# Kernel tuning notes

Hardware: AMD Instinct MI355X
Metric: run time of the kernel (lower is better)

Reference implementation:

```python
import jax, jax.numpy as jnp
import numpy as np

BATCH, FLAT_IN, PROJ_DIM, HEADS, ACT_DIM = 2048, 512, 256, 16384, 64


def setup_inputs() -> dict:
    key = jax.random.key(0)
    k1, k2, k3, k4 = jax.random.split(key, 4)
    state = jax.random.normal(k1, (BATCH, FLAT_IN), dtype=jnp.float32)
    random_projection = jax.random.normal(k2, (FLAT_IN, PROJ_DIM), dtype=jnp.float32)
    memories = jax.random.normal(k3, (HEADS, PROJ_DIM), dtype=jnp.float32)
    logits = jax.random.normal(k4, (HEADS, ACT_DIM), dtype=jnp.float32)
    return {"state": state, "random_projection": random_projection,
            "memories": memories, "logits": logits}


def reference(state, random_projection, memories, logits):
    # state: [B, flat_in] -> projected [B, proj_dim] (proj_dim branch of __call__)
    s = state.reshape(state.shape[0], -1) @ random_projection
    # sum(state[:,None] * memories[None,:], -1) == dot-product similarity GEMM
    similarities = jnp.einsum('bd,hd->bh', s, memories)  # [B, heads]
    closest = jnp.argmax(similarities, axis=1)           # [B]
    return logits[closest]                                # [B, act_dim]
```

## Files before the change

### kernel.cpp

```cpp
#include <hip/hip_runtime.h>

#define BATCH    2048
#define FLAT_IN  512
#define PROJ_DIM 256
#define HEADS    16384
#define ACT_DIM  64

typedef __attribute__((ext_vector_type(8))) short short8;
typedef _Float16 half8 __attribute__((ext_vector_type(8)));
typedef __attribute__((ext_vector_type(4))) float floatx4;

__device__ __forceinline__ unsigned short f2bf(float x) {
  unsigned u = __float_as_uint(x);
  u += 0x7fff + ((u >> 16) & 1);
  return (unsigned short)(u >> 16);
}
__device__ __forceinline__ float bf2f(unsigned short b) {
  return __uint_as_float(((unsigned)b) << 16);
}
__device__ __forceinline__ unsigned short f2h(float x) {
  _Float16 h = (_Float16)x;
  return __builtin_bit_cast(unsigned short, h);
}

__device__ __forceinline__ void top2_ins(float v, int h, float& b1, int& i1,
                                         float& b2, int& i2) {
  if (v > b1 || (v == b1 && h < i1)) { b2 = b1; i2 = i1; b1 = v; i1 = h; }
  else if (v > b2 || (v == b2 && h < i2)) { b2 = v; i2 = h; }
}

#define GLDS16(g, l)                                                          \
  __builtin_amdgcn_global_load_lds(                                           \
      (__attribute__((address_space(1))) void*)(void*)(g),                    \
      (__attribute__((address_space(3))) void*)(l), 16, 0, 0)

__global__ __launch_bounds__(256) void prep(
    const float* __restrict__ state, const float* __restrict__ rp,
    const float* __restrict__ mem,
    unsigned short* __restrict__ st_hi, unsigned short* __restrict__ st_mid,
    unsigned short* __restrict__ rpT_hi, unsigned short* __restrict__ rpT_mid,
    unsigned short* __restrict__ mem_f16)
{
  const int tid = threadIdx.x;
  const int b = blockIdx.x;
  if (b < 1024) {
    int i = b * 256 + tid;
    float4 v = ((const float4*)state)[i];
    ushort4 h, m;
    h.x = f2bf(v.x); m.x = f2bf(v.x - bf2f(h.x));
    h.y = f2bf(v.y); m.y = f2bf(v.y - bf2f(h.y));
    h.z = f2bf(v.z); m.z = f2bf(v.z - bf2f(h.z));
    h.w = f2bf(v.w); m.w = f2bf(v.w - bf2f(h.w));
    ((ushort4*)st_hi)[i]  = h;
    ((ushort4*)st_mid)[i] = m;
  } else if (b < 1056) {
    __shared__ float t[64][65];
    int bid = b - 1024;
    int k0 = (bid >> 2) * 64, n0 = (bid & 3) * 64;
#pragma unroll
    for (int it = 0; it < 16; ++it) {
      int lin = it * 256 + tid;
      int kr = lin >> 6, nc = lin & 63;
      t[kr][nc] = rp[(size_t)(k0 + kr) * PROJ_DIM + n0 + nc];
    }
    __syncthreads();
#pragma unroll
    for (int it = 0; it < 16; ++it) {
      int lin = it * 256 + tid;
      int nr = lin >> 6, kc = lin & 63;
      float v = t[kc][nr];
      unsigned short hh = f2bf(v);
      rpT_hi [(size_t)(n0 + nr) * FLAT_IN + k0 + kc] = hh;
      rpT_mid[(size_t)(n0 + nr) * FLAT_IN + k0 + kc] = f2bf(v - bf2f(hh));
    }
  } else {
    int i2 = (b - 1056) * 256 + tid;
    float4 x = ((const float4*)mem)[2 * i2];
    float4 y = ((const float4*)mem)[2 * i2 + 1];
    short8 o;
    o[0] = (short)f2h(x.x); o[1] = (short)f2h(x.y);
    o[2] = (short)f2h(x.z); o[3] = (short)f2h(x.w);
    o[4] = (short)f2h(y.x); o[5] = (short)f2h(y.y);
    o[6] = (short)f2h(y.z); o[7] = (short)f2h(y.w);
    ((short8*)mem_f16)[i2] = o;
  }
}

__global__ __launch_bounds__(256, 2) void gemm_proj(
    const unsigned short* __restrict__ Ahi, const unsigned short* __restrict__ Amid,
    const unsigned short* __restrict__ Bhi, const unsigned short* __restrict__ Bmid,
    float* __restrict__ S, unsigned short* __restrict__ Sf16)
{
  __shared__ __align__(16) unsigned short sm[4][64 * 64];
  const int tid = threadIdx.x;
  const int lane = tid & 63, w = tid >> 6;
  const int quad = lane >> 4, col = lane & 15;
  const int wm = (w >> 1) * 32, wn = (w & 1) * 32;
  const int m0 = blockIdx.x * 64, n0 = blockIdx.y * 64;

  floatx4 acc[2][2];
#pragma unroll
  for (int i = 0; i < 2; ++i)
#pragma unroll
    for (int j = 0; j < 2; ++j) {
      acc[i][j][0] = 0.f; acc[i][j][1] = 0.f;
      acc[i][j][2] = 0.f; acc[i][j][3] = 0.f;
    }

  const int P0 = tid, P1 = tid + 256;
  const int r0 = P0 >> 3, kl0 = (P0 & 7) ^ (r0 & 7);
  const int r1 = P1 >> 3, kl1 = (P1 & 7) ^ (r1 & 7);

  for (int kc = 0; kc < FLAT_IN; kc += 64) {
    GLDS16(Ahi  + (size_t)(m0 + r0) * FLAT_IN + kc + kl0 * 8, &sm[0][P0 * 8]);
    GLDS16(Ahi  + (size_t)(m0 + r1) * FLAT_IN + kc + kl1 * 8, &sm[0][P1 * 8]);
    GLDS16(Amid + (size_t)(m0 + r0) * FLAT_IN + kc + kl0 * 8, &sm[1][P0 * 8]);
    GLDS16(Amid + (size_t)(m0 + r1) * FLAT_IN + kc + kl1 * 8, &sm[1][P1 * 8]);
    GLDS16(Bhi  + (size_t)(n0 + r0) * FLAT_IN + kc + kl0 * 8, &sm[2][P0 * 8]);
    GLDS16(Bhi  + (size_t)(n0 + r1) * FLAT_IN + kc + kl1 * 8, &sm[2][P1 * 8]);
    GLDS16(Bmid + (size_t)(n0 + r0) * FLAT_IN + kc + kl0 * 8, &sm[3][P0 * 8]);
    GLDS16(Bmid + (size_t)(n0 + r1) * FLAT_IN + kc + kl1 * 8, &sm[3][P1 * 8]);
    __syncthreads();

#pragma unroll
    for (int ks = 0; ks < 2; ++ks) {
      short8 bf[2][2];
#pragma unroll
      for (int j = 0; j < 2; ++j) {
        int rr = wn + j * 16 + col;
        int off = rr * 64 + (((ks * 4 + quad) ^ (rr & 7)) * 8);
        bf[j][0] = *(const short8*)&sm[2][off];
        bf[j][1] = *(const short8*)&sm[3][off];
      }
#pragma unroll
      for (int i = 0; i < 2; ++i) {
        int rr = wm + i * 16 + col;
        int off = rr * 64 + (((ks * 4 + quad) ^ (rr & 7)) * 8);
        short8 a0 = *(const short8*)&sm[0][off];
        short8 a1 = *(const short8*)&sm[1][off];
#pragma unroll
        for (int j = 0; j < 2; ++j) {
          acc[i][j] = __builtin_amdgcn_mfma_f32_16x16x32_bf16(a0, bf[j][0], acc[i][j], 0, 0, 0);
          acc[i][j] = __builtin_amdgcn_mfma_f32_16x16x32_bf16(a0, bf[j][1], acc[i][j], 0, 0, 0);
          acc[i][j] = __builtin_amdgcn_mfma_f32_16x16x32_bf16(a1, bf[j][0], acc[i][j], 0, 0, 0);
        }
      }
    }
    __syncthreads();
  }

#pragma unroll
  for (int i = 0; i < 2; ++i)
#pragma unroll
    for (int j = 0; j < 2; ++j)
#pragma unroll
      for (int r = 0; r < 4; ++r) {
        int row = m0 + wm + i * 16 + quad * 4 + r;
        int c   = n0 + wn + j * 16 + col;
        float v = acc[i][j][r];
        S   [(size_t)row * PROJ_DIM + c] = v;
        Sf16[(size_t)row * PROJ_DIM + c] = f2h(v);
      }
}

__global__ __launch_bounds__(512, 4) void sim_topk(
    const unsigned short* __restrict__ Af16,
    const unsigned short* __restrict__ Bf16,
    float4* __restrict__ partial)
{
  __shared__ __align__(16) unsigned short smA[128 * 64];
  __shared__ __align__(16) unsigned short smB[256 * 64];
  const int tid = threadIdx.x;
  const int lane = tid & 63, w = tid >> 6;
  const int quad = lane >> 4, col = lane & 15;
  const int wm = (w >> 2) * 64, wn = (w & 3) * 64;
  const int m0 = blockIdx.x * 128;
  const int h0 = blockIdx.y * 256;

  floatx4 acc[4][4];
#pragma unroll
  for (int i = 0; i < 4; ++i)
#pragma unroll
    for (int j = 0; j < 4; ++j) {
      acc[i][j][0] = 0.f; acc[i][j][1] = 0.f;
      acc[i][j][2] = 0.f; acc[i][j][3] = 0.f;
    }

  const int PA0 = tid, PA1 = tid + 512;
  const int ra0 = PA0 >> 3, ka0 = (PA0 & 7) ^ (ra0 & 7);
  const int ra1 = PA1 >> 3, ka1 = (PA1 & 7) ^ (ra1 & 7);
  int rb[4], kb[4];
#pragma unroll
  for (int t = 0; t < 4; ++t) {
    int P = t * 512 + tid;
    rb[t] = P >> 3; kb[t] = (P & 7) ^ (rb[t] & 7);
  }

  for (int kc = 0; kc < PROJ_DIM; kc += 64) {
    GLDS16(Af16 + (size_t)(m0 + ra0) * PROJ_DIM + kc + ka0 * 8, &smA[PA0 * 8]);
    GLDS16(Af16 + (size_t)(m0 + ra1) * PROJ_DIM + kc + ka1 * 8, &smA[PA1 * 8]);
#pragma unroll
    for (int t = 0; t < 4; ++t) {
      GLDS16(Bf16 + (size_t)(h0 + rb[t]) * PROJ_DIM + kc + kb[t] * 8,
             &smB[(t * 512 + tid) * 8]);
    }
    __syncthreads();

#pragma unroll
    for (int ks = 0; ks < 2; ++ks) {
      half8 a[4], bfr[4];
#pragma unroll
      for (int i = 0; i < 4; ++i) {
        int rr = wm + i * 16 + col;
        int off = rr * 64 + (((ks * 4 + quad) ^ (rr & 7)) * 8);
        a[i] = *(const half8*)&smA[off];
      }
#pragma unroll
      for (int j = 0; j < 4; ++j) {
        int rr = wn + j * 16 + col;
        int off = rr * 64 + (((ks * 4 + quad) ^ (rr & 7)) * 8);
        bfr[j] = *(const half8*)&smB[off];
      }
#pragma unroll
      for (int i = 0; i < 4; ++i)
#pragma unroll
        for (int j = 0; j < 4; ++j)
          acc[i][j] = __builtin_amdgcn_mfma_f32_16x16x32_f16(a[i], bfr[j], acc[i][j], 0, 0, 0);
    }
    __syncthreads();
  }

  float4* lds_p = (float4*)smA;

#pragma unroll
  for (int i = 0; i < 4; ++i)
#pragma unroll
    for (int r = 0; r < 4; ++r) {
      float b1 = acc[i][0][r]; int h1 = h0 + wn + col;
      float b2 = -3.4e38f;     int h2 = h1;
#pragma unroll
      for (int j = 1; j < 4; ++j) {
        float v = acc[i][j][r]; int h = h0 + wn + j * 16 + col;
        if (v > b1) { b2 = b1; h2 = h1; b1 = v; h1 = h; }
        else if (v > b2) { b2 = v; h2 = h; }
      }
#pragma unroll
      for (int m = 1; m <= 8; m <<= 1) {
        float ob1 = __shfl_xor(b1, m); int oh1 = __shfl_xor(h1, m);
        float ob2 = __shfl_xor(b2, m); int oh2 = __shfl_xor(h2, m);
        if (ob1 > b1) {
          if (b1 > ob2) { b2 = b1;  h2 = h1;  }
          else          { b2 = ob2; h2 = oh2; }
          b1 = ob1; h1 = oh1;
        } else if (ob1 > b2) { b2 = ob1; h2 = oh1; }
      }
      if (col == 0) {
        int row = wm + i * 16 + quad * 4 + r;
        lds_p[row * 4 + (w & 3)] =
            make_float4(b1, __int_as_float(h1), b2, __int_as_float(h2));
      }
    }
  __syncthreads();

  if (tid < 128) {
    int row = tid;
    float b1 = -3.4e38f, b2 = -3.4e38f; int h1 = 0x7fffffff, h2 = 0x7fffffff;
#pragma unroll
    for (int t = 0; t < 4; ++t) {
      float4 p = lds_p[row * 4 + t];
      top2_ins(p.x, __float_as_int(p.y), b1, h1, b2, h2);
      top2_ins(p.z, __float_as_int(p.w), b1, h1, b2, h2);
    }
    partial[(size_t)(m0 + row) * 64 + blockIdx.y] =
        make_float4(b1, __int_as_float(h1), b2, __int_as_float(h2));
  }
}

__global__ __launch_bounds__(64) void finalize(
    const float4* __restrict__ partial, const float* __restrict__ S,
    const float* __restrict__ Mem, const float* __restrict__ logits,
    float* __restrict__ out)
{
  const int row  = blockIdx.x;
  const int lane = threadIdx.x;

  float4 p = partial[(size_t)row * 64 + lane];
  float v0 = p.x; int c0 = __float_as_int(p.y);
  float v1 = p.z; int c1 = __float_as_int(p.w);

  int cand[4];
#pragma unroll
  for (int t = 0; t < 4; ++t) {
    float lv; int lh;
    if (v0 > v1 || (v0 == v1 && c0 < c1)) { lv = v0; lh = c0; }
    else                                  { lv = v1; lh = c1; }
#pragma unroll
    for (int d = 32; d; d >>= 1) {
      float ov = __shfl_xor(lv, d); int oh = __shfl_xor(lh, d);
      if (ov > lv || (ov == lv && oh < lh)) { lv = ov; lh = oh; }
    }
    cand[t] = lh;
    if (c0 == lh) v0 = -3.4e38f;
    if (c1 == lh) v1 = -3.4e38f;
  }

  float4 sv = ((const float4*)(S + (size_t)row * PROJ_DIM))[lane];
  float bestv = -3.4e38f; int besth = 0x7fffffff;
#pragma unroll
  for (int t = 0; t < 4; ++t) {
    float4 mv = ((const float4*)(Mem + (size_t)cand[t] * PROJ_DIM))[lane];
    float d = sv.x * mv.x + sv.y * mv.y + sv.z * mv.z + sv.w * mv.w;
#pragma unroll
    for (int s = 32; s; s >>= 1) d += __shfl_xor(d, s);
    if (d > bestv || (d == bestv && cand[t] < besth)) { bestv = d; besth = cand[t]; }
  }
  out[(size_t)row * ACT_DIM + lane] = logits[(size_t)besth * ACT_DIM + lane];
}

extern "C" void kernel_launch(void* const* d_in, const int* in_sizes, int n_in,
                              void* d_out, int out_size, void* d_ws, size_t ws_size,
                              hipStream_t stream) {
  const float* state  = (const float*)d_in[0];
  const float* rp     = (const float*)d_in[1];
  const float* mem    = (const float*)d_in[2];
  const float* logits = (const float*)d_in[3];
  float* out = (float*)d_out;

  char* ws = (char*)d_ws;
  unsigned short* st_hi   = (unsigned short*)(ws);
  unsigned short* st_mid  = (unsigned short*)(ws + (2u  << 20));
  unsigned short* rpT_hi  = (unsigned short*)(ws + (4u  << 20));
  unsigned short* rpT_mid = (unsigned short*)(ws + (4u  << 20) + (256u << 10));
  unsigned short* mem_f16 = (unsigned short*)(ws + (8u  << 20));
  float*          s       = (float*)(ws + (16u << 20));
  unsigned short* s_f16   = (unsigned short*)(ws + (18u << 20));
  float4*         part    = (float4*)(ws + (20u << 20));

  prep<<<3104, 256, 0, stream>>>(state, rp, mem, st_hi, st_mid,
                                 rpT_hi, rpT_mid, mem_f16);

  gemm_proj<<<dim3(32, 4), 256, 0, stream>>>(st_hi, st_mid, rpT_hi, rpT_mid,
                                             s, s_f16);

  sim_topk<<<dim3(16, 64), 512, 0, stream>>>(s_f16, mem_f16, part);

  finalize<<<BATCH, 64, 0, stream>>>(part, s, mem, logits, out);
}
```

Before: 139.4 us.

## Fuse state split into projection GEMM and register-prefetch tiles in both GEMMs

The bf16 hi/mid split of the state matrix now happens inside gemm_proj, which loads fp32 state directly. This removes a prep pass and its 4 MB round trip through the workspace. Both GEMMs drop the direct global-to-LDS loads in favour of register prefetch of the next K tile overlapped with MFMA work, with a single LDS buffer and extra barriers. sim_topk moves from 512-thread 128x256 tiles to 256-thread 128x128 tiles with a transposed grid, so finalize now merges 128 partials per row instead of 64. This adds register pressure and conversion work inside the GEMM loop.

```diff
diff --git a/kernel.cpp b/kernel.cpp
--- a/kernel.cpp
+++ b/kernel.cpp
@@ -29,52 +29,15 @@
   else if (v > b2 || (v == b2 && h < i2)) { b2 = v; i2 = h; }
 }
 
-#define GLDS16(g, l)                                                          \
-  __builtin_amdgcn_global_load_lds(                                           \
-      (__attribute__((address_space(1))) void*)(void*)(g),                    \
-      (__attribute__((address_space(3))) void*)(l), 16, 0, 0)
-
 __global__ __launch_bounds__(256) void prep(
-    const float* __restrict__ state, const float* __restrict__ rp,
-    const float* __restrict__ mem,
-    unsigned short* __restrict__ st_hi, unsigned short* __restrict__ st_mid,
+    const float* __restrict__ rp, const float* __restrict__ mem,
     unsigned short* __restrict__ rpT_hi, unsigned short* __restrict__ rpT_mid,
     unsigned short* __restrict__ mem_f16)
 {
   const int tid = threadIdx.x;
   const int b = blockIdx.x;
-  if (b < 1024) {
-    int i = b * 256 + tid;
-    float4 v = ((const float4*)state)[i];
-    ushort4 h, m;
-    h.x = f2bf(v.x); m.x = f2bf(v.x - bf2f(h.x));
-    h.y = f2bf(v.y); m.y = f2bf(v.y - bf2f(h.y));
-    h.z = f2bf(v.z); m.z = f2bf(v.z - bf2f(h.z));
-    h.w = f2bf(v.w); m.w = f2bf(v.w - bf2f(h.w));
-    ((ushort4*)st_hi)[i]  = h;
-    ((ushort4*)st_mid)[i] = m;
-  } else if (b < 1056) {
-    __shared__ float t[64][65];
-    int bid = b - 1024;
-    int k0 = (bid >> 2) * 64, n0 = (bid & 3) * 64;
-#pragma unroll
-    for (int it = 0; it < 16; ++it) {
-      int lin = it * 256 + tid;
-      int kr = lin >> 6, nc = lin & 63;
-      t[kr][nc] = rp[(size_t)(k0 + kr) * PROJ_DIM + n0 + nc];
-    }
-    __syncthreads();
-#pragma unroll
-    for (int it = 0; it < 16; ++it) {
-      int lin = it * 256 + tid;
-      int nr = lin >> 6, kc = lin & 63;
-      float v = t[kc][nr];
-      unsigned short hh = f2bf(v);
-      rpT_hi [(size_t)(n0 + nr) * FLAT_IN + k0 + kc] = hh;
-      rpT_mid[(size_t)(n0 + nr) * FLAT_IN + k0 + kc] = f2bf(v - bf2f(hh));
-    }
-  } else {
-    int i2 = (b - 1056) * 256 + tid;
+  if (b < 2048) {
+    int i2 = b * 256 + tid;
     float4 x = ((const float4*)mem)[2 * i2];
     float4 y = ((const float4*)mem)[2 * i2 + 1];
     short8 o;
@@ -83,15 +46,38 @@
     o[4] = (short)f2h(y.x); o[5] = (short)f2h(y.y);
     o[6] = (short)f2h(y.z); o[7] = (short)f2h(y.w);
     ((short8*)mem_f16)[i2] = o;
-  }
-}
-
-__global__ __launch_bounds__(256, 2) void gemm_proj(
-    const unsigned short* __restrict__ Ahi, const unsigned short* __restrict__ Amid,
+  } else {
+    __shared__ float t[64][65];
+    int bid = b - 2048;
+    int k0 = (bid >> 2) * 64, n0 = (bid & 3) * 64;
+#pragma unroll
+    for (int it = 0; it < 16; ++it) {
+      int lin = it * 256 + tid;
+      int kr = lin >> 6, nc = lin & 63;
+      t[kr][nc] = rp[(size_t)(k0 + kr) * PROJ_DIM + n0 + nc];
+    }
+    __syncthreads();
+#pragma unroll
+    for (int it = 0; it < 16; ++it) {
+      int lin = it * 256 + tid;
+      int nr = lin >> 6, kc = lin & 63;
+      float v = t[kc][nr];
+      unsigned short hh = f2bf(v);
+      rpT_hi [(size_t)(n0 + nr) * FLAT_IN + k0 + kc] = hh;
+      rpT_mid[(size_t)(n0 + nr) * FLAT_IN + k0 + kc] = f2bf(v - bf2f(hh));
+    }
+  }
+}
+
+__global__ __launch_bounds__(256, 3) void gemm_proj(
+    const float* __restrict__ state,
     const unsigned short* __restrict__ Bhi, const unsigned short* __restrict__ Bmid,
     float* __restrict__ S, unsigned short* __restrict__ Sf16)
 {
-  __shared__ __align__(16) unsigned short sm[4][64 * 64];
+  __shared__ __align__(16) unsigned short smAhi [64 * 64];
+  __shared__ __align__(16) unsigned short smAmid[64 * 64];
+  __shared__ __align__(16) unsigned short smBhi [64 * 64];
+  __shared__ __align__(16) unsigned short smBmid[64 * 64];
   const int tid = threadIdx.x;
   const int lane = tid & 63, w = tid >> 6;
   const int quad = lane >> 4, col = lane & 15;
@@ -111,17 +97,45 @@
   const int r0 = P0 >> 3, kl0 = (P0 & 7) ^ (r0 & 7);
   const int r1 = P1 >> 3, kl1 = (P1 & 7) ^ (r1 & 7);
 
-  for (int kc = 0; kc < FLAT_IN; kc += 64) {
-    GLDS16(Ahi  + (size_t)(m0 + r0) * FLAT_IN + kc + kl0 * 8, &sm[0][P0 * 8]);
-    GLDS16(Ahi  + (size_t)(m0 + r1) * FLAT_IN + kc + kl1 * 8, &sm[0][P1 * 8]);
-    GLDS16(Amid + (size_t)(m0 + r0) * FLAT_IN + kc + kl0 * 8, &sm[1][P0 * 8]);
-    GLDS16(Amid + (size_t)(m0 + r1) * FLAT_IN + kc + kl1 * 8, &sm[1][P1 * 8]);
-    GLDS16(Bhi  + (size_t)(n0 + r0) * FLAT_IN + kc + kl0 * 8, &sm[2][P0 * 8]);
-    GLDS16(Bhi  + (size_t)(n0 + r1) * FLAT_IN + kc + kl1 * 8, &sm[2][P1 * 8]);
-    GLDS16(Bmid + (size_t)(n0 + r0) * FLAT_IN + kc + kl0 * 8, &sm[3][P0 * 8]);
-    GLDS16(Bmid + (size_t)(n0 + r1) * FLAT_IN + kc + kl1 * 8, &sm[3][P1 * 8]);
-    __syncthreads();
-
+  float4 pa[2][2];
+  float4 pbh[2], pbm[2];
+
+  auto gload = [&](int kc) {
+    const float* a0 = state + (size_t)(m0 + r0) * FLAT_IN + kc + kl0 * 8;
+    const float* a1 = state + (size_t)(m0 + r1) * FLAT_IN + kc + kl1 * 8;
+    pa[0][0] = *(const float4*)a0; pa[0][1] = *(const float4*)(a0 + 4);
+    pa[1][0] = *(const float4*)a1; pa[1][1] = *(const float4*)(a1 + 4);
+    pbh[0] = *(const float4*)(Bhi  + (size_t)(n0 + r0) * FLAT_IN + kc + kl0 * 8);
+    pbh[1] = *(const float4*)(Bhi  + (size_t)(n0 + r1) * FLAT_IN + kc + kl1 * 8);
+    pbm[0] = *(const float4*)(Bmid + (size_t)(n0 + r0) * FLAT_IN + kc + kl0 * 8);
+    pbm[1] = *(const float4*)(Bmid + (size_t)(n0 + r1) * FLAT_IN + kc + kl1 * 8);
+  };
+  auto swrite = [&]() {
+#pragma unroll
+    for (int t = 0; t < 2; ++t) {
+      int P = t ? P1 : P0;
+      float f[8] = {pa[t][0].x, pa[t][0].y, pa[t][0].z, pa[t][0].w,
+                    pa[t][1].x, pa[t][1].y, pa[t][1].z, pa[t][1].w};
+      short8 vh, vm;
+#pragma unroll
+      for (int q = 0; q < 8; ++q) {
+        unsigned short hh = f2bf(f[q]);
+        vh[q] = (short)hh;
+        vm[q] = (short)f2bf(f[q] - bf2f(hh));
+      }
+      *(short8*)&smAhi [P * 8] = vh;
+      *(short8*)&smAmid[P * 8] = vm;
+      *(float4*)&smBhi [P * 8] = pbh[t];
+      *(float4*)&smBmid[P * 8] = pbm[t];
+    }
+  };
+
+  gload(0);
+  swrite();
+  __syncthreads();
+
+  for (int it = 0; it < 8; ++it) {
+    if (it < 7) gload((it + 1) * 64);
 #pragma unroll
     for (int ks = 0; ks < 2; ++ks) {
       short8 bf[2][2];
@@ -129,15 +143,15 @@
       for (int j = 0; j < 2; ++j) {
         int rr = wn + j * 16 + col;
         int off = rr * 64 + (((ks * 4 + quad) ^ (rr & 7)) * 8);
-        bf[j][0] = *(const short8*)&sm[2][off];
-        bf[j][1] = *(const short8*)&sm[3][off];
+        bf[j][0] = *(const short8*)&smBhi [off];
+        bf[j][1] = *(const short8*)&smBmid[off];
       }
 #pragma unroll
       for (int i = 0; i < 2; ++i) {
         int rr = wm + i * 16 + col;
         int off = rr * 64 + (((ks * 4 + quad) ^ (rr & 7)) * 8);
-        short8 a0 = *(const short8*)&sm[0][off];
-        short8 a1 = *(const short8*)&sm[1][off];
+        short8 a0 = *(const short8*)&smAhi [off];
+        short8 a1 = *(const short8*)&smAmid[off];
 #pragma unroll
         for (int j = 0; j < 2; ++j) {
           acc[i][j] = __builtin_amdgcn_mfma_f32_16x16x32_bf16(a0, bf[j][0], acc[i][j], 0, 0, 0);
@@ -147,6 +161,7 @@
       }
     }
     __syncthreads();
+    if (it < 7) { swrite(); __syncthreads(); }
   }
 
 #pragma unroll
@@ -163,19 +178,19 @@
       }
 }
 
-__global__ __launch_bounds__(512, 4) void sim_topk(
+__global__ __launch_bounds__(256, 3) void sim_topk(
     const unsigned short* __restrict__ Af16,
     const unsigned short* __restrict__ Bf16,
     float4* __restrict__ partial)
 {
   __shared__ __align__(16) unsigned short smA[128 * 64];
-  __shared__ __align__(16) unsigned short smB[256 * 64];
+  __shared__ __align__(16) unsigned short smB[128 * 64];
   const int tid = threadIdx.x;
   const int lane = tid & 63, w = tid >> 6;
   const int quad = lane >> 4, col = lane & 15;
-  const int wm = (w >> 2) * 64, wn = (w & 3) * 64;
-  const int m0 = blockIdx.x * 128;
-  const int h0 = blockIdx.y * 256;
+  const int wm = (w >> 1) * 64, wn = (w & 1) * 64;
+  const int h0 = blockIdx.x * 128;
+  const int m0 = blockIdx.y * 128;
 
   floatx4 acc[4][4];
 #pragma unroll
@@ -186,40 +201,48 @@
       acc[i][j][2] = 0.f; acc[i][j][3] = 0.f;
     }
 
-  const int PA0 = tid, PA1 = tid + 512;
-  const int ra0 = PA0 >> 3, ka0 = (PA0 & 7) ^ (ra0 & 7);
-  const int ra1 = PA1 >> 3, ka1 = (PA1 & 7) ^ (ra1 & 7);
-  int rb[4], kb[4];
+  int rA[4], kA[4];
 #pragma unroll
   for (int t = 0; t < 4; ++t) {
-    int P = t * 512 + tid;
-    rb[t] = P >> 3; kb[t] = (P & 7) ^ (rb[t] & 7);
-  }
-
-  for (int kc = 0; kc < PROJ_DIM; kc += 64) {
-    GLDS16(Af16 + (size_t)(m0 + ra0) * PROJ_DIM + kc + ka0 * 8, &smA[PA0 * 8]);
-    GLDS16(Af16 + (size_t)(m0 + ra1) * PROJ_DIM + kc + ka1 * 8, &smA[PA1 * 8]);
+    int P = t * 256 + tid;
+    rA[t] = P >> 3; kA[t] = (P & 7) ^ (rA[t] & 7);
+  }
+
+  float4 pa[4], pb[4];
+  auto gload = [&](int kc) {
+#pragma unroll
+    for (int t = 0; t < 4; ++t)
+      pa[t] = *(const float4*)(Af16 + (size_t)(m0 + rA[t]) * PROJ_DIM + kc + kA[t] * 8);
+#pragma unroll
+    for (int t = 0; t < 4; ++t)
+      pb[t] = *(const float4*)(Bf16 + (size_t)(h0 + rA[t]) * PROJ_DIM + kc + kA[t] * 8);
+  };
+  auto swrite = [&]() {
 #pragma unroll
     for (int t = 0; t < 4; ++t) {
-      GLDS16(Bf16 + (size_t)(h0 + rb[t]) * PROJ_DIM + kc + kb[t] * 8,
-             &smB[(t * 512 + tid) * 8]);
-    }
-    __syncthreads();
-
+      *(float4*)&smA[(t * 256 + tid) * 8] = pa[t];
+      *(float4*)&smB[(t * 256 + tid) * 8] = pb[t];
+    }
+  };
+
+  gload(0);
+  swrite();
+  __syncthreads();
+
+  for (int it = 0; it < 4; ++it) {
+    if (it < 3) gload((it + 1) * 64);
 #pragma unroll
     for (int ks = 0; ks < 2; ++ks) {
       half8 a[4], bfr[4];
 #pragma unroll
       for (int i = 0; i < 4; ++i) {
         int rr = wm + i * 16 + col;
-        int off = rr * 64 + (((ks * 4 + quad) ^ (rr & 7)) * 8);
-        a[i] = *(const half8*)&smA[off];
+        a[i] = *(const half8*)&smA[rr * 64 + (((ks * 4 + quad) ^ (rr & 7)) * 8)];
       }
 #pragma unroll
       for (int j = 0; j < 4; ++j) {
         int rr = wn + j * 16 + col;
-        int off = rr * 64 + (((ks * 4 + quad) ^ (rr & 7)) * 8);
-        bfr[j] = *(const half8*)&smB[off];
+        bfr[j] = *(const half8*)&smB[rr * 64 + (((ks * 4 + quad) ^ (rr & 7)) * 8)];
       }
 #pragma unroll
       for (int i = 0; i < 4; ++i)
@@ -228,6 +251,7 @@
           acc[i][j] = __builtin_amdgcn_mfma_f32_16x16x32_f16(a[i], bfr[j], acc[i][j], 0, 0, 0);
     }
     __syncthreads();
+    if (it < 3) { swrite(); __syncthreads(); }
   }
 
   float4* lds_p = (float4*)smA;
@@ -256,7 +280,7 @@
       }
       if (col == 0) {
         int row = wm + i * 16 + quad * 4 + r;
-        lds_p[row * 4 + (w & 3)] =
+        lds_p[row * 2 + (w & 1)] =
             make_float4(b1, __int_as_float(h1), b2, __int_as_float(h2));
       }
     }
@@ -264,14 +288,13 @@
 
   if (tid < 128) {
     int row = tid;
-    float b1 = -3.4e38f, b2 = -3.4e38f; int h1 = 0x7fffffff, h2 = 0x7fffffff;
-#pragma unroll
-    for (int t = 0; t < 4; ++t) {
-      float4 p = lds_p[row * 4 + t];
-      top2_ins(p.x, __float_as_int(p.y), b1, h1, b2, h2);
-      top2_ins(p.z, __float_as_int(p.w), b1, h1, b2, h2);
-    }
-    partial[(size_t)(m0 + row) * 64 + blockIdx.y] =
+    float4 px = lds_p[row * 2 + 0];
+    float4 py = lds_p[row * 2 + 1];
+    float b1 = px.x; int h1 = __float_as_int(px.y);
+    float b2 = px.z; int h2 = __float_as_int(px.w);
+    top2_ins(py.x, __float_as_int(py.y), b1, h1, b2, h2);
+    top2_ins(py.z, __float_as_int(py.w), b1, h1, b2, h2);
+    partial[(size_t)(m0 + row) * 128 + blockIdx.x] =
         make_float4(b1, __int_as_float(h1), b2, __int_as_float(h2));
   }
 }
@@ -284,24 +307,28 @@
   const int row  = blockIdx.x;
   const int lane = threadIdx.x;
 
-  float4 p = partial[(size_t)row * 64 + lane];
-  float v0 = p.x; int c0 = __float_as_int(p.y);
-  float v1 = p.z; int c1 = __float_as_int(p.w);
+  float4 p0 = partial[(size_t)row * 128 + lane];
+  float4 p1 = partial[(size_t)row * 128 + 64 + lane];
+  float v[4] = {p0.x, p0.z, p1.x, p1.z};
+  int   c[4] = {__float_as_int(p0.y), __float_as_int(p0.w),
+                __float_as_int(p1.y), __float_as_int(p1.w)};
 
   int cand[4];
 #pragma unroll
   for (int t = 0; t < 4; ++t) {
-    float lv; int lh;
-    if (v0 > v1 || (v0 == v1 && c0 < c1)) { lv = v0; lh = c0; }
-    else                                  { lv = v1; lh = c1; }
+    float lv = v[0]; int lh = c[0];
+#pragma unroll
+    for (int q = 1; q < 4; ++q)
+      if (v[q] > lv || (v[q] == lv && c[q] < lh)) { lv = v[q]; lh = c[q]; }
 #pragma unroll
     for (int d = 32; d; d >>= 1) {
       float ov = __shfl_xor(lv, d); int oh = __shfl_xor(lh, d);
       if (ov > lv || (ov == lv && oh < lh)) { lv = ov; lh = oh; }
     }
     cand[t] = lh;
-    if (c0 == lh) v0 = -3.4e38f;
-    if (c1 == lh) v1 = -3.4e38f;
+#pragma unroll
+    for (int q = 0; q < 4; ++q)
+      if (c[q] == lh) v[q] = -3.4e38f;
   }
 
   float4 sv = ((const float4*)(S + (size_t)row * PROJ_DIM))[lane];
@@ -327,22 +354,18 @@
   float* out = (float*)d_out;
 
   char* ws = (char*)d_ws;
-  unsigned short* st_hi   = (unsigned short*)(ws);
-  unsigned short* st_mid  = (unsigned short*)(ws + (2u  << 20));
-  unsigned short* rpT_hi  = (unsigned short*)(ws + (4u  << 20));
-  unsigned short* rpT_mid = (unsigned short*)(ws + (4u  << 20) + (256u << 10));
-  unsigned short* mem_f16 = (unsigned short*)(ws + (8u  << 20));
-  float*          s       = (float*)(ws + (16u << 20));
-  unsigned short* s_f16   = (unsigned short*)(ws + (18u << 20));
-  float4*         part    = (float4*)(ws + (20u << 20));
-
-  prep<<<3104, 256, 0, stream>>>(state, rp, mem, st_hi, st_mid,
-                                 rpT_hi, rpT_mid, mem_f16);
-
-  gemm_proj<<<dim3(32, 4), 256, 0, stream>>>(st_hi, st_mid, rpT_hi, rpT_mid,
-                                             s, s_f16);
-
-  sim_topk<<<dim3(16, 64), 512, 0, stream>>>(s_f16, mem_f16, part);
+  unsigned short* rpT_hi  = (unsigned short*)(ws);
+  unsigned short* rpT_mid = (unsigned short*)(ws + (256u << 10));
+  unsigned short* mem_f16 = (unsigned short*)(ws + (1u  << 20));
+  float*          s       = (float*)(ws + (9u  << 20));
+  unsigned short* s_f16   = (unsigned short*)(ws + (11u << 20));
+  float4*         part    = (float4*)(ws + (12u << 20));
+
+  prep<<<2080, 256, 0, stream>>>(rp, mem, rpT_hi, rpT_mid, mem_f16);
+
+  gemm_proj<<<dim3(32, 4), 256, 0, stream>>>(state, rpT_hi, rpT_mid, s, s_f16);
+
+  sim_topk<<<dim3(128, 16), 256, 0, stream>>>(s_f16, mem_f16, part);
 
   finalize<<<BATCH, 64, 0, stream>>>(part, s, mem, logits, out);
 }
```

Measured after the change: 204.3 us. 1.47x slower.

## Load full-K tiles once in sim_topk with 128x128 tiles and 256 threads

Applied to the files above, without the earlier changes.

The similarity GEMM now loads the entire K=256 extent of a 128-row A tile and a 128-row memory tile into LDS in one pass, which removes the per-K-chunk loop and its barriers. The tile shape goes from 128x256 with 512 threads to 128x128 with 256 threads. The grid is reordered so that blocks sharing the same memory tile run together. The partial top-2 buffer grows to 128 entries per row, and finalize now merges four candidates per lane. The 128 KB of LDS per block limits occupancy to about one block per CU and leaves no overlap between loads and MFMA work.

```diff
diff --git a/kernel.cpp b/kernel.cpp
--- a/kernel.cpp
+++ b/kernel.cpp
@@ -163,19 +163,34 @@
       }
 }
 
-__global__ __launch_bounds__(512, 4) void sim_topk(
+__global__ __launch_bounds__(256, 1) void sim_topk(
     const unsigned short* __restrict__ Af16,
     const unsigned short* __restrict__ Bf16,
     float4* __restrict__ partial)
 {
-  __shared__ __align__(16) unsigned short smA[128 * 64];
-  __shared__ __align__(16) unsigned short smB[256 * 64];
+  __shared__ __align__(16) unsigned short smA[128 * 256];
+  __shared__ __align__(16) unsigned short smB[128 * 256];
   const int tid = threadIdx.x;
   const int lane = tid & 63, w = tid >> 6;
   const int quad = lane >> 4, col = lane & 15;
-  const int wm = (w >> 2) * 64, wn = (w & 3) * 64;
-  const int m0 = blockIdx.x * 128;
-  const int h0 = blockIdx.y * 256;
+  const int wm = (w >> 1) * 64, wn = (w & 1) * 64;
+  const int h0 = blockIdx.x * 128;
+  const int m0 = blockIdx.y * 128;
+
+#pragma unroll
+  for (int t = 0; t < 16; ++t) {
+    int P = t * 256 + tid;
+    int row = P >> 5;
+    int sl  = (P & 31) ^ (row & 31);
+    GLDS16(Af16 + (size_t)(m0 + row) * PROJ_DIM + sl * 8, &smA[P * 8]);
+  }
+#pragma unroll
+  for (int t = 0; t < 16; ++t) {
+    int P = t * 256 + tid;
+    int row = P >> 5;
+    int sl  = (P & 31) ^ (row & 31);
+    GLDS16(Bf16 + (size_t)(h0 + row) * PROJ_DIM + sl * 8, &smB[P * 8]);
+  }
 
   floatx4 acc[4][4];
 #pragma unroll
@@ -186,49 +201,30 @@
       acc[i][j][2] = 0.f; acc[i][j][3] = 0.f;
     }
 
-  const int PA0 = tid, PA1 = tid + 512;
-  const int ra0 = PA0 >> 3, ka0 = (PA0 & 7) ^ (ra0 & 7);
-  const int ra1 = PA1 >> 3, ka1 = (PA1 & 7) ^ (ra1 & 7);
-  int rb[4], kb[4];
-#pragma unroll
-  for (int t = 0; t < 4; ++t) {
-    int P = t * 512 + tid;
-    rb[t] = P >> 3; kb[t] = (P & 7) ^ (rb[t] & 7);
-  }
-
-  for (int kc = 0; kc < PROJ_DIM; kc += 64) {
-    GLDS16(Af16 + (size_t)(m0 + ra0) * PROJ_DIM + kc + ka0 * 8, &smA[PA0 * 8]);
-    GLDS16(Af16 + (size_t)(m0 + ra1) * PROJ_DIM + kc + ka1 * 8, &smA[PA1 * 8]);
-#pragma unroll
-    for (int t = 0; t < 4; ++t) {
-      GLDS16(Bf16 + (size_t)(h0 + rb[t]) * PROJ_DIM + kc + kb[t] * 8,
-             &smB[(t * 512 + tid) * 8]);
-    }
-    __syncthreads();
-
-#pragma unroll
-    for (int ks = 0; ks < 2; ++ks) {
-      half8 a[4], bfr[4];
-#pragma unroll
-      for (int i = 0; i < 4; ++i) {
-        int rr = wm + i * 16 + col;
-        int off = rr * 64 + (((ks * 4 + quad) ^ (rr & 7)) * 8);
-        a[i] = *(const half8*)&smA[off];
-      }
-#pragma unroll
-      for (int j = 0; j < 4; ++j) {
-        int rr = wn + j * 16 + col;
-        int off = rr * 64 + (((ks * 4 + quad) ^ (rr & 7)) * 8);
-        bfr[j] = *(const half8*)&smB[off];
-      }
-#pragma unroll
-      for (int i = 0; i < 4; ++i)
-#pragma unroll
-        for (int j = 0; j < 4; ++j)
-          acc[i][j] = __builtin_amdgcn_mfma_f32_16x16x32_f16(a[i], bfr[j], acc[i][j], 0, 0, 0);
-    }
-    __syncthreads();
-  }
+  __syncthreads();
+
+#pragma unroll
+  for (int ks = 0; ks < 8; ++ks) {
+    half8 a[4], bfr[4];
+#pragma unroll
+    for (int i = 0; i < 4; ++i) {
+      int rr = wm + i * 16 + col;
+      int phys = (ks * 4 + quad) ^ (rr & 31);
+      a[i] = *(const half8*)&smA[rr * 256 + phys * 8];
+    }
+#pragma unroll
+    for (int j = 0; j < 4; ++j) {
+      int rr = wn + j * 16 + col;
+      int phys = (ks * 4 + quad) ^ (rr & 31);
+      bfr[j] = *(const half8*)&smB[rr * 256 + phys * 8];
+    }
+#pragma unroll
+    for (int i = 0; i < 4; ++i)
+#pragma unroll
+      for (int j = 0; j < 4; ++j)
+        acc[i][j] = __builtin_amdgcn_mfma_f32_16x16x32_f16(a[i], bfr[j], acc[i][j], 0, 0, 0);
+  }
+  __syncthreads();
 
   float4* lds_p = (float4*)smA;
 
@@ -256,7 +252,7 @@
       }
       if (col == 0) {
         int row = wm + i * 16 + quad * 4 + r;
-        lds_p[row * 4 + (w & 3)] =
+        lds_p[row * 2 + (w & 1)] =
             make_float4(b1, __int_as_float(h1), b2, __int_as_float(h2));
       }
     }
@@ -264,14 +260,13 @@
 
   if (tid < 128) {
     int row = tid;
-    float b1 = -3.4e38f, b2 = -3.4e38f; int h1 = 0x7fffffff, h2 = 0x7fffffff;
-#pragma unroll
-    for (int t = 0; t < 4; ++t) {
-      float4 p = lds_p[row * 4 + t];
-      top2_ins(p.x, __float_as_int(p.y), b1, h1, b2, h2);
-      top2_ins(p.z, __float_as_int(p.w), b1, h1, b2, h2);
-    }
-    partial[(size_t)(m0 + row) * 64 + blockIdx.y] =
+    float4 px = lds_p[row * 2 + 0];
+    float4 py = lds_p[row * 2 + 1];
+    float b1 = px.x; int h1 = __float_as_int(px.y);
+    float b2 = px.z; int h2 = __float_as_int(px.w);
+    top2_ins(py.x, __float_as_int(py.y), b1, h1, b2, h2);
+    top2_ins(py.z, __float_as_int(py.w), b1, h1, b2, h2);
+    partial[(size_t)(m0 + row) * 128 + blockIdx.x] =
         make_float4(b1, __int_as_float(h1), b2, __int_as_float(h2));
   }
 }
@@ -284,24 +279,28 @@
   const int row  = blockIdx.x;
   const int lane = threadIdx.x;
 
-  float4 p = partial[(size_t)row * 64 + lane];
-  float v0 = p.x; int c0 = __float_as_int(p.y);
-  float v1 = p.z; int c1 = __float_as_int(p.w);
+  float4 p0 = partial[(size_t)row * 128 + lane];
+  float4 p1 = partial[(size_t)row * 128 + 64 + lane];
+  float v[4] = {p0.x, p0.z, p1.x, p1.z};
+  int   c[4] = {__float_as_int(p0.y), __float_as_int(p0.w),
+                __float_as_int(p1.y), __float_as_int(p1.w)};
 
   int cand[4];
 #pragma unroll
   for (int t = 0; t < 4; ++t) {
-    float lv; int lh;
-    if (v0 > v1 || (v0 == v1 && c0 < c1)) { lv = v0; lh = c0; }
-    else                                  { lv = v1; lh = c1; }
+    float lv = v[0]; int lh = c[0];
+#pragma unroll
+    for (int q = 1; q < 4; ++q)
+      if (v[q] > lv || (v[q] == lv && c[q] < lh)) { lv = v[q]; lh = c[q]; }
 #pragma unroll
     for (int d = 32; d; d >>= 1) {
       float ov = __shfl_xor(lv, d); int oh = __shfl_xor(lh, d);
       if (ov > lv || (ov == lv && oh < lh)) { lv = ov; lh = oh; }
     }
     cand[t] = lh;
-    if (c0 == lh) v0 = -3.4e38f;
-    if (c1 == lh) v1 = -3.4e38f;
+#pragma unroll
+    for (int q = 0; q < 4; ++q)
+      if (c[q] == lh) v[q] = -3.4e38f;
   }
 
   float4 sv = ((const float4*)(S + (size_t)row * PROJ_DIM))[lane];
@@ -342,7 +341,7 @@
   gemm_proj<<<dim3(32, 4), 256, 0, stream>>>(st_hi, st_mid, rpT_hi, rpT_mid,
                                              s, s_f16);
 
-  sim_topk<<<dim3(16, 64), 512, 0, stream>>>(s_f16, mem_f16, part);
+  sim_topk<<<dim3(128, 16), 256, 0, stream>>>(s_f16, mem_f16, part);
 
   finalize<<<BATCH, 64, 0, stream>>>(part, s, mem, logits, out);
 }
```

Measured after the change: 194.8 us. 1.4x slower.

## Move memory fp16 conversion into projection GEMM, simplify top-k epilogue

Applied to the files above, without the earlier changes.

The memories fp32→fp16 conversion moves from the prep kernel into the projection GEMM launch as extra blocks, so the small 128-block GEMM runs alongside conversion work instead of after it. The sim_topk epilogue drops the per-block top-2 LDS merge and its barrier. Each wave now writes its own top-1 candidate per row, giving four candidates per head chunk for finalize. The sim_topk grid is transposed so consecutive blocks share the same memory chunk, and finalize reads four times as many partials to rebuild its candidate list.

```diff
diff --git a/kernel.cpp b/kernel.cpp
--- a/kernel.cpp
+++ b/kernel.cpp
@@ -23,12 +23,6 @@
   return __builtin_bit_cast(unsigned short, h);
 }
 
-__device__ __forceinline__ void top2_ins(float v, int h, float& b1, int& i1,
-                                         float& b2, int& i2) {
-  if (v > b1 || (v == b1 && h < i1)) { b2 = b1; i2 = i1; b1 = v; i1 = h; }
-  else if (v > b2 || (v == b2 && h < i2)) { b2 = v; i2 = h; }
-}
-
 #define GLDS16(g, l)                                                          \
   __builtin_amdgcn_global_load_lds(                                           \
       (__attribute__((address_space(1))) void*)(void*)(g),                    \
@@ -36,10 +30,8 @@
 
 __global__ __launch_bounds__(256) void prep(
     const float* __restrict__ state, const float* __restrict__ rp,
-    const float* __restrict__ mem,
     unsigned short* __restrict__ st_hi, unsigned short* __restrict__ st_mid,
-    unsigned short* __restrict__ rpT_hi, unsigned short* __restrict__ rpT_mid,
-    unsigned short* __restrict__ mem_f16)
+    unsigned short* __restrict__ rpT_hi, unsigned short* __restrict__ rpT_mid)
 {
   const int tid = threadIdx.x;
   const int b = blockIdx.x;
@@ -53,7 +45,7 @@
     h.w = f2bf(v.w); m.w = f2bf(v.w - bf2f(h.w));
     ((ushort4*)st_hi)[i]  = h;
     ((ushort4*)st_mid)[i] = m;
-  } else if (b < 1056) {
+  } else {
     __shared__ float t[64][65];
     int bid = b - 1024;
     int k0 = (bid >> 2) * 64, n0 = (bid & 3) * 64;
@@ -73,8 +65,19 @@
       rpT_hi [(size_t)(n0 + nr) * FLAT_IN + k0 + kc] = hh;
       rpT_mid[(size_t)(n0 + nr) * FLAT_IN + k0 + kc] = f2bf(v - bf2f(hh));
     }
-  } else {
-    int i2 = (b - 1056) * 256 + tid;
+  }
+}
+
+__global__ __launch_bounds__(256, 2) void gemm_conv(
+    const unsigned short* __restrict__ Ahi, const unsigned short* __restrict__ Amid,
+    const unsigned short* __restrict__ Bhi, const unsigned short* __restrict__ Bmid,
+    const float* __restrict__ mem,
+    float* __restrict__ S, unsigned short* __restrict__ Sf16,
+    unsigned short* __restrict__ mem_f16)
+{
+  const int tid = threadIdx.x;
+  if (blockIdx.x >= 128) {
+    int i2 = (blockIdx.x - 128) * 256 + tid;
     float4 x = ((const float4*)mem)[2 * i2];
     float4 y = ((const float4*)mem)[2 * i2 + 1];
     short8 o;
@@ -83,20 +86,15 @@
     o[4] = (short)f2h(y.x); o[5] = (short)f2h(y.y);
     o[6] = (short)f2h(y.z); o[7] = (short)f2h(y.w);
     ((short8*)mem_f16)[i2] = o;
-  }
-}
-
-__global__ __launch_bounds__(256, 2) void gemm_proj(
-    const unsigned short* __restrict__ Ahi, const unsigned short* __restrict__ Amid,
-    const unsigned short* __restrict__ Bhi, const unsigned short* __restrict__ Bmid,
-    float* __restrict__ S, unsigned short* __restrict__ Sf16)
-{
+    return;
+  }
+
   __shared__ __align__(16) unsigned short sm[4][64 * 64];
-  const int tid = threadIdx.x;
   const int lane = tid & 63, w = tid >> 6;
   const int quad = lane >> 4, col = lane & 15;
   const int wm = (w >> 1) * 32, wn = (w & 1) * 32;
-  const int m0 = blockIdx.x * 64, n0 = blockIdx.y * 64;
+  const int g = blockIdx.x;
+  const int m0 = (g & 31) * 64, n0 = (g >> 5) * 64;
 
   floatx4 acc[2][2];
 #pragma unroll
@@ -166,7 +164,7 @@
 __global__ __launch_bounds__(512, 4) void sim_topk(
     const unsigned short* __restrict__ Af16,
     const unsigned short* __restrict__ Bf16,
-    float4* __restrict__ partial)
+    float2* __restrict__ part2)
 {
   __shared__ __align__(16) unsigned short smA[128 * 64];
   __shared__ __align__(16) unsigned short smB[256 * 64];
@@ -174,8 +172,9 @@
   const int lane = tid & 63, w = tid >> 6;
   const int quad = lane >> 4, col = lane & 15;
   const int wm = (w >> 2) * 64, wn = (w & 3) * 64;
-  const int m0 = blockIdx.x * 128;
-  const int h0 = blockIdx.y * 256;
+  const int hc = blockIdx.x;
+  const int h0 = hc * 256;
+  const int m0 = blockIdx.y * 128;
 
   floatx4 acc[4][4];
 #pragma unroll
@@ -230,78 +229,60 @@
     __syncthreads();
   }
 
-  float4* lds_p = (float4*)smA;
-
 #pragma unroll
   for (int i = 0; i < 4; ++i)
 #pragma unroll
     for (int r = 0; r < 4; ++r) {
       float b1 = acc[i][0][r]; int h1 = h0 + wn + col;
-      float b2 = -3.4e38f;     int h2 = h1;
 #pragma unroll
       for (int j = 1; j < 4; ++j) {
         float v = acc[i][j][r]; int h = h0 + wn + j * 16 + col;
-        if (v > b1) { b2 = b1; h2 = h1; b1 = v; h1 = h; }
-        else if (v > b2) { b2 = v; h2 = h; }
+        if (v > b1) { b1 = v; h1 = h; }
       }
 #pragma unroll
       for (int m = 1; m <= 8; m <<= 1) {
-        float ob1 = __shfl_xor(b1, m); int oh1 = __shfl_xor(h1, m);
-        float ob2 = __shfl_xor(b2, m); int oh2 = __shfl_xor(h2, m);
-        if (ob1 > b1) {
-          if (b1 > ob2) { b2 = b1;  h2 = h1;  }
-          else          { b2 = ob2; h2 = oh2; }
-          b1 = ob1; h1 = oh1;
-        } else if (ob1 > b2) { b2 = ob1; h2 = oh1; }
+        float ob = __shfl_xor(b1, m); int oh = __shfl_xor(h1, m);
+        if (ob > b1 || (ob == b1 && oh < h1)) { b1 = ob; h1 = oh; }
       }
       if (col == 0) {
-        int row = wm + i * 16 + quad * 4 + r;
-        lds_p[row * 4 + (w & 3)] =
-            make_float4(b1, __int_as_float(h1), b2, __int_as_float(h2));
-      }
-    }
-  __syncthreads();
-
-  if (tid < 128) {
-    int row = tid;
-    float b1 = -3.4e38f, b2 = -3.4e38f; int h1 = 0x7fffffff, h2 = 0x7fffffff;
-#pragma unroll
-    for (int t = 0; t < 4; ++t) {
-      float4 p = lds_p[row * 4 + t];
-      top2_ins(p.x, __float_as_int(p.y), b1, h1, b2, h2);
-      top2_ins(p.z, __float_as_int(p.w), b1, h1, b2, h2);
-    }
-    partial[(size_t)(m0 + row) * 64 + blockIdx.y] =
-        make_float4(b1, __int_as_float(h1), b2, __int_as_float(h2));
-  }
+        int row = m0 + wm + i * 16 + quad * 4 + r;
+        part2[((size_t)row * 64 + hc) * 4 + (w & 3)] =
+            make_float2(b1, __int_as_float(h1));
+      }
+    }
 }
 
 __global__ __launch_bounds__(64) void finalize(
-    const float4* __restrict__ partial, const float* __restrict__ S,
+    const float2* __restrict__ part2, const float* __restrict__ S,
     const float* __restrict__ Mem, const float* __restrict__ logits,
     float* __restrict__ out)
 {
   const int row  = blockIdx.x;
   const int lane = threadIdx.x;
 
-  float4 p = partial[(size_t)row * 64 + lane];
-  float v0 = p.x; int c0 = __float_as_int(p.y);
-  float v1 = p.z; int c1 = __float_as_int(p.w);
+  float v[4]; int c[4];
+#pragma unroll
+  for (int t = 0; t < 4; ++t) {
+    float2 p = part2[(size_t)row * 256 + t * 64 + lane];
+    v[t] = p.x; c[t] = __float_as_int(p.y);
+  }
 
   int cand[4];
 #pragma unroll
   for (int t = 0; t < 4; ++t) {
-    float lv; int lh;
-    if (v0 > v1 || (v0 == v1 && c0 < c1)) { lv = v0; lh = c0; }
-    else                                  { lv = v1; lh = c1; }
+    float lv = v[0]; int lh = c[0];
+#pragma unroll
+    for (int q = 1; q < 4; ++q)
+      if (v[q] > lv || (v[q] == lv && c[q] < lh)) { lv = v[q]; lh = c[q]; }
 #pragma unroll
     for (int d = 32; d; d >>= 1) {
       float ov = __shfl_xor(lv, d); int oh = __shfl_xor(lh, d);
       if (ov > lv || (ov == lv && oh < lh)) { lv = ov; lh = oh; }
     }
     cand[t] = lh;
-    if (c0 == lh) v0 = -3.4e38f;
-    if (c1 == lh) v1 = -3.4e38f;
+#pragma unroll
+    for (int q = 0; q < 4; ++q)
+      if (c[q] == lh) v[q] = -3.4e38f;
   }
 
   float4 sv = ((const float4*)(S + (size_t)row * PROJ_DIM))[lane];
@@ -334,15 +315,14 @@
   unsigned short* mem_f16 = (unsigned short*)(ws + (8u  << 20));
   float*          s       = (float*)(ws + (16u << 20));
   unsigned short* s_f16   = (unsigned short*)(ws + (18u << 20));
-  float4*         part    = (float4*)(ws + (20u << 20));
-
-  prep<<<3104, 256, 0, stream>>>(state, rp, mem, st_hi, st_mid,
-                                 rpT_hi, rpT_mid, mem_f16);
-
-  gemm_proj<<<dim3(32, 4), 256, 0, stream>>>(st_hi, st_mid, rpT_hi, rpT_mid,
-                                             s, s_f16);
-
-  sim_topk<<<dim3(16, 64), 512, 0, stream>>>(s_f16, mem_f16, part);
-
-  finalize<<<BATCH, 64, 0, stream>>>(part, s, mem, logits, out);
-}
+  float2*         part2   = (float2*)(ws + (20u << 20));
+
+  prep<<<1056, 256, 0, stream>>>(state, rp, st_hi, st_mid, rpT_hi, rpT_mid);
+
+  gemm_conv<<<2176, 256, 0, stream>>>(st_hi, st_mid, rpT_hi, rpT_mid, mem,
+                                      s, s_f16, mem_f16);
+
+  sim_topk<<<dim3(64, 16), 512, 0, stream>>>(s_f16, mem_f16, part2);
+
+  finalize<<<BATCH, 64, 0, stream>>>(part2, s, mem, logits, out);
+}
```

Result: faster. 120.7 us (-13.4%).
